# Optimization experiments

Measured on AMD Instinct MI355X. Metric: run time of the kernel, lower is better.

## Reference

```python
import jax, jax.numpy as jnp
import numpy as np

EPS = 1e-8


def setup_inputs() -> dict:
    key = jax.random.key(0)
    k1, k2, k3 = jax.random.split(key, 3)
    B, K, L, D = 4, 64, 128, 768
    context = jax.random.normal(k1, (B, K, 2, L, D), dtype=jnp.float32)
    # MlpModule(input_size=D): Linear(D, D) -> ReLU -> Linear(D, 1)
    w1 = jax.random.normal(k2, (D, D), dtype=jnp.float32) * (1.0 / np.sqrt(D))
    b1 = jnp.zeros((D,), dtype=jnp.float32)
    w2 = jax.random.normal(k3, (D, 1), dtype=jnp.float32) * (1.0 / np.sqrt(D))
    b2 = jnp.zeros((1,), dtype=jnp.float32)
    return {"context": context, "w1": w1, "b1": b1, "w2": w2, "b2": b2}


def reference(context, w1, b1, w2, b2):
    # context: [B, K, 2, L, D]; slice 0 = context tokens, slice 1 = entity tokens
    ctx = context[:, :, 0, :, :]   # [B, K, L, D]
    ent = context[:, :, 1, :, :]   # [B, K, L, D]

    ctx_norm = jnp.linalg.norm(ctx, axis=-1, keepdims=True)  # [B, K, L, 1]
    ent_norm = jnp.linalg.norm(ent, axis=-1, keepdims=True)  # [B, K, L, 1]

    # cosine-similarity score matrix: [B, K, L, L]
    denom = ctx_norm * jnp.swapaxes(ent_norm, -1, -2) + EPS
    scores = jnp.einsum('bkld,bkmd->bklm', ctx, ent) / denom

    # normalized embeddings (torch code does in-place /= before the stack)
    ctx_n = ctx / ctx_norm
    ent_n = ent / ent_norm

    # top-1 match along entity axis, gather matched entity token per context token
    argmax_idx = jnp.argmax(scores, axis=-1)                       # [B, K, L] int
    matched = jnp.take_along_axis(ent_n, argmax_idx[..., None], axis=2)  # [B, K, L, D]

    pair = jnp.stack([ctx_n, matched], axis=-2)  # [B, K, L, 2, D]

    # MLP: Linear(D,D) -> ReLU -> Linear(D,1), then sum over the pair axis
    h = jax.nn.relu(jnp.einsum('bklpd,de->bklpe', pair, w1) + b1)
    out = jnp.einsum('bklpd,do->bklpo', h, w2) + b2   # [B, K, L, 2, 1]
    out = jnp.sum(out, axis=-2)                        # [B, K, L, 1]
    return jnp.squeeze(out, axis=-1)                   # [B, K, L]
```

## Files before the change

kernel.cpp:

```cpp
#include <hip/hip_runtime.h>
#include <hip/hip_bf16.h>
#include <stdint.h>

#define NB 4
#define NK 64
#define NL 128
#define ND 768
#define NBK (NB*NK)
#define NROW (NBK*NL)
#define LD2 (NL*ND)
#define EPSF 1e-8f
#define THETA 2e-3f
#define CAP 16384
#define BTS 56

typedef __bf16 bf16x8 __attribute__((ext_vector_type(8)));
typedef float  f32x4  __attribute__((ext_vector_type(4)));

__device__ __forceinline__ int row_off(int r) {
  if (r < NROW) return r*ND + (r >> 7)*LD2;
  int r2 = r - NROW;
  return r2*ND + (r2 >> 7)*LD2 + LD2;
}

__global__ __launch_bounds__(256) void k0_w1t(const float* __restrict__ w1,
                                              __bf16* __restrict__ w1t,
                                              unsigned long long* __restrict__ amax2,
                                              unsigned* __restrict__ cntg) {
  __shared__ float tile[64][68];
  int idx = blockIdx.x*256 + threadIdx.x;
  if (idx < NROW) amax2[idx] = 0ull;
  if (idx == 0) *cntg = 0u;
  int kb = (blockIdx.x / 12) * 64, eb = (blockIdx.x % 12) * 64;
  int t = threadIdx.x;
  int r = t >> 2, c0 = (t & 3) * 16;
  #pragma unroll
  for (int j = 0; j < 4; j++) {
    f32x4 v = *(const f32x4*)(w1 + (kb + r)*ND + eb + c0 + j*4);
    *(f32x4*)&tile[r][c0 + j*4] = v;
  }
  __syncthreads();
  int e = t & 63, gi = t >> 6;
  int eg = eb + e;
  #pragma unroll
  for (int g2 = 0; g2 < 2; g2++) {
    int g = gi*2 + g2;
    bf16x8 o;
    #pragma unroll
    for (int j = 0; j < 8; j++) o[j] = (__bf16)tile[g*8 + j][e];
    int G = (kb >> 3) + (g ^ (eg & 7));
    *(bf16x8*)(w1t + eg*ND + G*8) = o;
  }
}

__device__ __forceinline__ void cvt4(f32x4 v, unsigned& hp0, unsigned& hp1,
                                     unsigned& lp0, unsigned& lp1, float& sq) {
  unsigned u0 = __float_as_uint(v[0]), u1 = __float_as_uint(v[1]);
  unsigned u2 = __float_as_uint(v[2]), u3 = __float_as_uint(v[3]);
  hp0 = (u1 & 0xffff0000u) | (u0 >> 16);
  hp1 = (u3 & 0xffff0000u) | (u2 >> 16);
  float l0 = v[0] - __uint_as_float(u0 & 0xffff0000u);
  float l1 = v[1] - __uint_as_float(u1 & 0xffff0000u);
  float l2 = v[2] - __uint_as_float(u2 & 0xffff0000u);
  float l3 = v[3] - __uint_as_float(u3 & 0xffff0000u);
  lp0 = (__float_as_uint(l1) & 0xffff0000u) | (__float_as_uint(l0) >> 16);
  lp1 = (__float_as_uint(l3) & 0xffff0000u) | (__float_as_uint(l2) >> 16);
  sq += v[0]*v[0] + v[1]*v[1] + v[2]*v[2] + v[3]*v[3];
}

__global__ __launch_bounds__(256) void k2a_screen(
    const float* __restrict__ ctxall, float* __restrict__ norm,
    int* __restrict__ amax, unsigned* __restrict__ cntg,
    unsigned* __restrict__ list) {
  __shared__ alignas(16) __bf16 Ah[2][64*32], Al[2][64*32];
  __shared__ alignas(16) __bf16 Bh[2][128*BTS], Bl[2][128*BTS];
  __shared__ float einv_s[128];
  int bk = blockIdx.x & 255, half = blockIdx.x >> 8;
  int t = threadIdx.x;
  int w = t >> 6, lane = t & 63, quad = lane >> 4, eloc = lane & 15;
  bool hasA = (t < 128);
  int srow = t >> 1, kh = (t & 1) * 16;
  const float* asrc = ctxall + bk*2*LD2 + (half*64 + srow)*ND + kh;
  const float* bsrc = ctxall + bk*2*LD2 + LD2 + srow*ND + kh;

  f32x4 pa[4], pb[4];
  #pragma unroll
  for (int i = 0; i < 4; i++) pb[i] = *(const f32x4*)(bsrc + i*4);
  if (hasA) {
    #pragma unroll
    for (int i = 0; i < 4; i++) pa[i] = *(const f32x4*)(asrc + i*4);
  }
  float sqa = 0.f, sqb = 0.f;
  f32x4 acc[8];
  #pragma unroll
  for (int ct = 0; ct < 8; ct++) acc[ct] = (f32x4){0,0,0,0};

  int p = 0;
  for (int kt = 0; kt < 24; kt++) {
    unsigned h0,h1,h2,h3, l0,l1,l2,l3;
    cvt4(pb[0], h0, h1, l0, l1, sqb);
    cvt4(pb[1], h2, h3, l2, l3, sqb);
    *(uint4*)&Bh[p][srow*BTS + kh] = make_uint4(h0,h1,h2,h3);
    *(uint4*)&Bl[p][srow*BTS + kh] = make_uint4(l0,l1,l2,l3);
    cvt4(pb[2], h0, h1, l0, l1, sqb);
    cvt4(pb[3], h2, h3, l2, l3, sqb);
    *((uint4*)&Bh[p][srow*BTS + kh] + 1) = make_uint4(h0,h1,h2,h3);
    *((uint4*)&Bl[p][srow*BTS + kh] + 1) = make_uint4(l0,l1,l2,l3);
    if (hasA) {
      cvt4(pa[0], h0, h1, l0, l1, sqa);
      cvt4(pa[1], h2, h3, l2, l3, sqa);
      *(uint4*)&Ah[p][srow*32 + kh] = make_uint4(h0,h1,h2,h3);
      *(uint4*)&Al[p][srow*32 + kh] = make_uint4(l0,l1,l2,l3);
      cvt4(pa[2], h0, h1, l0, l1, sqa);
      cvt4(pa[3], h2, h3, l2, l3, sqa);
      *((uint4*)&Ah[p][srow*32 + kh] + 1) = make_uint4(h0,h1,h2,h3);
      *((uint4*)&Al[p][srow*32 + kh] + 1) = make_uint4(l0,l1,l2,l3);
    }
    __syncthreads();
    if (kt < 23) {
      const float* b2 = bsrc + (kt+1)*32;
      #pragma unroll
      for (int i = 0; i < 4; i++) pb[i] = *(const f32x4*)(b2 + i*4);
      if (hasA) {
        const float* a2 = asrc + (kt+1)*32;
        #pragma unroll
        for (int i = 0; i < 4; i++) pa[i] = *(const f32x4*)(a2 + i*4);
      }
    }
    bf16x8 ah = *(const bf16x8*)&Ah[p][(w*16+eloc)*32 + quad*8];
    bf16x8 al = *(const bf16x8*)&Al[p][(w*16+eloc)*32 + quad*8];
    #pragma unroll
    for (int ct = 0; ct < 8; ct++) {
      bf16x8 bh = *(const bf16x8*)&Bh[p][(ct*16+eloc)*BTS + quad*8];
      bf16x8 bl = *(const bf16x8*)&Bl[p][(ct*16+eloc)*BTS + quad*8];
      acc[ct] = __builtin_amdgcn_mfma_f32_16x16x32_bf16(al, bh, acc[ct], 0, 0, 0);
      acc[ct] = __builtin_amdgcn_mfma_f32_16x16x32_bf16(ah, bl, acc[ct], 0, 0, 0);
      acc[ct] = __builtin_amdgcn_mfma_f32_16x16x32_bf16(ah, bh, acc[ct], 0, 0, 0);
    }
    p ^= 1;
  }

  float stb = sqb + __shfl_xor(sqb, 1);
  if ((t & 1) == 0) {
    float n = sqrtf(stb);
    norm[NROW + bk*NL + srow] = n;
    einv_s[srow] = 1.0f / n;
  }
  if (hasA) {
    float sta = sqa + __shfl_xor(sqa, 1);
    if ((t & 1) == 0) norm[bk*NL + half*64 + srow] = sqrtf(sta);
  }
  __syncthreads();

  #pragma unroll
  for (int rr = 0; rr < 4; rr++) {
    float sc[8];
    float best = -3.0e38f; int bcol = 0;
    #pragma unroll
    for (int ct = 0; ct < 8; ct++) {
      sc[ct] = acc[ct][rr] * einv_s[ct*16 + eloc];
      int col = ct*16 + eloc;
      if (sc[ct] > best) { best = sc[ct]; bcol = col; }
    }
    #pragma unroll
    for (int m = 1; m < 16; m <<= 1) {
      float ov = __shfl_xor(best, m);
      int   oc = __shfl_xor(bcol, m);
      if (ov > best || (ov == best && oc < bcol)) { best = ov; bcol = oc; }
    }
    int grow = bk*NL + half*64 + w*16 + quad*4 + rr;
    if (eloc == 0) amax[grow] = bcol;
    int cnt = 0;
    #pragma unroll
    for (int ct = 0; ct < 8; ct++) cnt += (sc[ct] >= best - THETA) ? 1 : 0;
    #pragma unroll
    for (int m = 1; m < 16; m <<= 1) cnt += __shfl_xor(cnt, m);
    if (cnt >= 2) {
      #pragma unroll
      for (int ct = 0; ct < 8; ct++) {
        if (sc[ct] >= best - THETA) {
          unsigned idx = atomicAdd(cntg, 1u);
          if (idx < CAP) list[idx] = ((unsigned)grow << 7) | (unsigned)(ct*16 + eloc);
        }
      }
    }
  }
}

__global__ __launch_bounds__(256) void k2b_rescore(
    const float* __restrict__ ctxall, const float* __restrict__ norm,
    const unsigned* __restrict__ cntg, const unsigned* __restrict__ list,
    unsigned long long* __restrict__ amax2) {
  unsigned n = *cntg; if (n > CAP) n = CAP;
  int lane = threadIdx.x & 63;
  unsigned wv = blockIdx.x*4 + (threadIdx.x >> 6);
  for (unsigned e = wv; e < n; e += 256) {
    unsigned ent = list[e];
    int row = (int)(ent >> 7), col = (int)(ent & 127);
    int bk = row >> 7;
    const float* a = ctxall + row_off(row);
    const float* b = ctxall + bk*2*LD2 + LD2 + col*ND;
    float d = 0.f;
    #pragma unroll
    for (int i = 0; i < 3; i++) {
      f32x4 va = *(const f32x4*)(a + lane*12 + i*4);
      f32x4 vb = *(const f32x4*)(b + lane*12 + i*4);
      d += va[0]*vb[0] + va[1]*vb[1] + va[2]*vb[2] + va[3]*vb[3];
    }
    #pragma unroll
    for (int m = 1; m < 64; m <<= 1) d += __shfl_xor(d, m);
    if (lane == 0) {
      float cn = norm[row], en = norm[NROW + bk*NL + col];
      float s = d / (cn*en + EPSF);
      unsigned su = __float_as_uint(s);
      unsigned ord = (su & 0x80000000u) ? ~su : (su | 0x80000000u);
      unsigned long long key = ((unsigned long long)ord << 32) | (unsigned)(127 - col);
      atomicMax(&amax2[row], key);
    }
  }
}

__global__ __launch_bounds__(256, 2) void k3_mlp(
    const float* __restrict__ ctxall, const float* __restrict__ norm,
    const __bf16* __restrict__ w1t, const float* __restrict__ b1,
    const float* __restrict__ w2, float* __restrict__ val) {
  __shared__ alignas(16) __bf16 btile[2][16*768];
  int tid = threadIdx.x;
  int wave = tid >> 6, lane = tid & 63;
  int quad = lane >> 4, eloc = lane & 15;
  int rbase = blockIdx.x*128 + wave*32;

  #pragma unroll
  for (int i = 0; i < 6; i++) {
    __builtin_amdgcn_global_load_lds(
      (const __attribute__((address_space(1))) unsigned int*)(w1t + (i*256 + tid)*8),
      (__attribute__((address_space(3))) unsigned int*)(&btile[0][0] + (i*256 + tid)*8),
      16, 0, 0);
  }

  bf16x8 afrag[2][24];
  #pragma unroll
  for (int s = 0; s < 2; s++) {
    int r = rbase + s*16 + eloc;
    const float* src = ctxall + row_off(r);
    float rinv = 1.0f / norm[r];
    #pragma unroll
    for (int ks = 0; ks < 24; ks++) {
      const float* sp = src + ks*32 + quad*8;
      f32x4 v0 = *(const f32x4*)sp;
      f32x4 v1 = *(const f32x4*)(sp + 4);
      bf16x8 a;
      a[0] = (__bf16)(v0[0]*rinv); a[1] = (__bf16)(v0[1]*rinv);
      a[2] = (__bf16)(v0[2]*rinv); a[3] = (__bf16)(v0[3]*rinv);
      a[4] = (__bf16)(v1[0]*rinv); a[5] = (__bf16)(v1[1]*rinv);
      a[6] = (__bf16)(v1[2]*rinv); a[7] = (__bf16)(v1[3]*rinv);
      afrag[s][ks] = a;
    }
  }

  float oacc[2][4] = {{0,0,0,0},{0,0,0,0}};
  int p = 0;
  for (int nt = 0; nt < 48; nt++) {
    __syncthreads();
    if (nt < 47) {
      const __bf16* gsrc = w1t + (nt+1)*16*ND;
      #pragma unroll
      for (int i = 0; i < 6; i++) {
        __builtin_amdgcn_global_load_lds(
          (const __attribute__((address_space(1))) unsigned int*)(gsrc + (i*256 + tid)*8),
          (__attribute__((address_space(3))) unsigned int*)(&btile[p^1][0] + (i*256 + tid)*8),
          16, 0, 0);
      }
    }
    f32x4 h0 = {0,0,0,0}, h1 = {0,0,0,0};
    #pragma unroll
    for (int ks = 0; ks < 24; ks++) {
      int g = ks*4 + quad;
      bf16x8 bfrag = *(const bf16x8*)(&btile[p][0] + eloc*ND + ((g ^ (eloc & 7))*8));
      h0 = __builtin_amdgcn_mfma_f32_16x16x32_bf16(afrag[0][ks], bfrag, h0, 0, 0, 0);
      h1 = __builtin_amdgcn_mfma_f32_16x16x32_bf16(afrag[1][ks], bfrag, h1, 0, 0, 0);
    }
    float b1v = b1[nt*16 + eloc];
    float w2v = w2[nt*16 + eloc];
    #pragma unroll
    for (int rr = 0; rr < 4; rr++) {
      oacc[0][rr] += fmaxf(h0[rr] + b1v, 0.f) * w2v;
      oacc[1][rr] += fmaxf(h1[rr] + b1v, 0.f) * w2v;
    }
    p ^= 1;
  }
  #pragma unroll
  for (int m = 1; m < 16; m <<= 1)
    #pragma unroll
    for (int s = 0; s < 2; s++)
      #pragma unroll
      for (int rr = 0; rr < 4; rr++)
        oacc[s][rr] += __shfl_xor(oacc[s][rr], m);
  if (eloc == 0) {
    #pragma unroll
    for (int s = 0; s < 2; s++)
      #pragma unroll
      for (int rr = 0; rr < 4; rr++)
        val[rbase + s*16 + quad*4 + rr] = oacc[s][rr];
  }
}

__global__ void k4_out(const float* __restrict__ val, const int* __restrict__ amax,
                       const unsigned long long* __restrict__ amax2,
                       const float* __restrict__ b2, float* __restrict__ out) {
  int i = blockIdx.x*256 + threadIdx.x;
  int bk = i >> 7;
  unsigned long long k = amax2[i];
  int a = k ? (127 - (int)(k & 127ull)) : amax[i];
  out[i] = val[i] + val[NROW + bk*NL + a] + 2.0f*b2[0];
}

extern "C" void kernel_launch(void* const* d_in, const int* in_sizes, int n_in,
                              void* d_out, int out_size, void* d_ws, size_t ws_size,
                              hipStream_t stream) {
  const float* ctxall = (const float*)d_in[0];
  const float* w1 = (const float*)d_in[1];
  const float* b1 = (const float*)d_in[2];
  const float* w2 = (const float*)d_in[3];
  const float* b2 = (const float*)d_in[4];
  float* out = (float*)d_out;

  char* ws = (char*)d_ws;
  float*    norm = (float*)ws;
  int*      amax = (int*)(ws + 262144);
  float*    val  = (float*)(ws + 393216);
  __bf16*   w1t  = (__bf16*)(ws + 655360);
  unsigned long long* amax2 = (unsigned long long*)(ws + 1835008);
  unsigned* cntg = (unsigned*)(ws + 2097152);
  unsigned* list = (unsigned*)(ws + 2097156);

  hipLaunchKernelGGL(k0_w1t,     dim3(144),        dim3(256), 0, stream, w1, w1t, amax2, cntg);
  hipLaunchKernelGGL(k2a_screen, dim3(2*NBK),      dim3(256), 0, stream, ctxall, norm, amax, cntg, list);
  hipLaunchKernelGGL(k2b_rescore,dim3(64),         dim3(256), 0, stream, ctxall, norm, cntg, list, amax2);
  hipLaunchKernelGGL(k3_mlp,     dim3(2*NROW/128), dim3(256), 0, stream, ctxall, norm, w1t, b1, w2, val);
  hipLaunchKernelGGL(k4_out,     dim3(NROW/256),   dim3(256), 0, stream, val, amax, amax2, b2, out);
}
```

Measured before the change: 393.6 us.

## Fuse context-row MLP into screening kernel to reuse staged context tiles

The screening kernel grows to 512 threads and, while it stages context rows in LDS for the cosine screen, also runs the first MLP layer for those context rows. It uses a pre-fragmented bf16 copy of W1 that k0 now also writes, and finishes ReLU and the W2 reduction in the same kernel. The standalone MLP kernel then only processes the matched/entity half of rows, so each context row is read from global memory once instead of twice. In exchange the fused kernel carries far more accumulators and register pressure, fetches W1 fragments from global every k-step in every block, and the LDS row stride changes to 40.

```diff
diff --git a/kernel.cpp b/kernel.cpp
--- a/kernel.cpp
+++ b/kernel.cpp
@@ -12,7 +12,7 @@
 #define EPSF 1e-8f
 #define THETA 2e-3f
 #define CAP 16384
-#define BTS 56
+#define TSTR 40
 
 typedef __bf16 bf16x8 __attribute__((ext_vector_type(8)));
 typedef float  f32x4  __attribute__((ext_vector_type(4)));
@@ -25,6 +25,7 @@
 
 __global__ __launch_bounds__(256) void k0_w1t(const float* __restrict__ w1,
                                               __bf16* __restrict__ w1t,
+                                              __bf16* __restrict__ w1f,
                                               unsigned long long* __restrict__ amax2,
                                               unsigned* __restrict__ cntg) {
   __shared__ float tile[64][68];
@@ -50,6 +51,19 @@
     for (int j = 0; j < 8; j++) o[j] = (__bf16)tile[g*8 + j][e];
     int G = (kb >> 3) + (g ^ (eg & 7));
     *(bf16x8*)(w1t + eg*ND + G*8) = o;
+  }
+  #pragma unroll
+  for (int rr = 0; rr < 2; rr++) {
+    int task = t + rr*256;
+    int fi = task >> 6, l = task & 63;
+    int nt_loc = fi & 3, ks_loc = fi >> 2;
+    int quad = l >> 4, eloc = l & 15;
+    bf16x8 o;
+    #pragma unroll
+    for (int j = 0; j < 8; j++)
+      o[j] = (__bf16)tile[ks_loc*32 + quad*8 + j][nt_loc*16 + eloc];
+    int nt = (eb >> 4) + nt_loc, ks = (kb >> 5) + ks_loc;
+    *(bf16x8*)(w1f + (size_t)((nt*24 + ks)*64 + l)*8) = o;
   }
 }
 
@@ -68,122 +82,196 @@
   sq += v[0]*v[0] + v[1]*v[1] + v[2]*v[2] + v[3]*v[3];
 }
 
-__global__ __launch_bounds__(256) void k2a_screen(
+__global__ __launch_bounds__(512, 2) void k2m_fused(
     const float* __restrict__ ctxall, float* __restrict__ norm,
     int* __restrict__ amax, unsigned* __restrict__ cntg,
-    unsigned* __restrict__ list) {
-  __shared__ alignas(16) __bf16 Ah[2][64*32], Al[2][64*32];
-  __shared__ alignas(16) __bf16 Bh[2][128*BTS], Bl[2][128*BTS];
+    unsigned* __restrict__ list, const __bf16* __restrict__ w1f,
+    const float* __restrict__ b1, const float* __restrict__ w2,
+    float* __restrict__ val) {
+  __shared__ alignas(16) __bf16 Bh[2][128*TSTR], Bl[2][128*TSTR];
+  __shared__ alignas(16) __bf16 Ah[2][64*TSTR],  Al[2][64*TSTR];
   __shared__ float einv_s[128];
+  __shared__ float cinv_s[64];
+  __shared__ float red[8][64];
   int bk = blockIdx.x & 255, half = blockIdx.x >> 8;
   int t = threadIdx.x;
   int w = t >> 6, lane = t & 63, quad = lane >> 4, eloc = lane & 15;
-  bool hasA = (t < 128);
-  int srow = t >> 1, kh = (t & 1) * 16;
-  const float* asrc = ctxall + bk*2*LD2 + (half*64 + srow)*ND + kh;
+  bool stE = (t < 256);
+  bool stC = (t >= 256 && t < 384);
+  int srow  = (t >> 1) & 127;
+  int csrow = (t >> 1) & 63;
+  int kh = (t & 1) * 16;
   const float* bsrc = ctxall + bk*2*LD2 + LD2 + srow*ND + kh;
+  const float* asrc = ctxall + bk*2*LD2 + (half*64 + csrow)*ND + kh;
 
   f32x4 pa[4], pb[4];
-  #pragma unroll
-  for (int i = 0; i < 4; i++) pb[i] = *(const f32x4*)(bsrc + i*4);
-  if (hasA) {
+  if (stE) {
+    #pragma unroll
+    for (int i = 0; i < 4; i++) pb[i] = *(const f32x4*)(bsrc + i*4);
+  } else if (stC) {
     #pragma unroll
     for (int i = 0; i < 4; i++) pa[i] = *(const f32x4*)(asrc + i*4);
   }
   float sqa = 0.f, sqb = 0.f;
-  f32x4 acc[8];
-  #pragma unroll
-  for (int ct = 0; ct < 8; ct++) acc[ct] = (f32x4){0,0,0,0};
+  f32x4 accs[8];
+  #pragma unroll
+  for (int ct = 0; ct < 8; ct++) accs[ct] = (f32x4){0,0,0,0};
+  f32x4 accm[6][4];
+  #pragma unroll
+  for (int i = 0; i < 6; i++)
+    #pragma unroll
+    for (int rt = 0; rt < 4; rt++) accm[i][rt] = (f32x4){0,0,0,0};
+  float b1v[6], w2v[6];
+  #pragma unroll
+  for (int i = 0; i < 6; i++) {
+    int c = (w*6 + i)*16 + eloc;
+    b1v[i] = b1[c];
+    w2v[i] = w2[c];
+  }
 
   int p = 0;
   for (int kt = 0; kt < 24; kt++) {
     unsigned h0,h1,h2,h3, l0,l1,l2,l3;
-    cvt4(pb[0], h0, h1, l0, l1, sqb);
-    cvt4(pb[1], h2, h3, l2, l3, sqb);
-    *(uint4*)&Bh[p][srow*BTS + kh] = make_uint4(h0,h1,h2,h3);
-    *(uint4*)&Bl[p][srow*BTS + kh] = make_uint4(l0,l1,l2,l3);
-    cvt4(pb[2], h0, h1, l0, l1, sqb);
-    cvt4(pb[3], h2, h3, l2, l3, sqb);
-    *((uint4*)&Bh[p][srow*BTS + kh] + 1) = make_uint4(h0,h1,h2,h3);
-    *((uint4*)&Bl[p][srow*BTS + kh] + 1) = make_uint4(l0,l1,l2,l3);
-    if (hasA) {
+    if (stE) {
+      cvt4(pb[0], h0, h1, l0, l1, sqb);
+      cvt4(pb[1], h2, h3, l2, l3, sqb);
+      *(uint4*)&Bh[p][srow*TSTR + kh] = make_uint4(h0,h1,h2,h3);
+      *(uint4*)&Bl[p][srow*TSTR + kh] = make_uint4(l0,l1,l2,l3);
+      cvt4(pb[2], h0, h1, l0, l1, sqb);
+      cvt4(pb[3], h2, h3, l2, l3, sqb);
+      *((uint4*)&Bh[p][srow*TSTR + kh] + 1) = make_uint4(h0,h1,h2,h3);
+      *((uint4*)&Bl[p][srow*TSTR + kh] + 1) = make_uint4(l0,l1,l2,l3);
+    } else if (stC) {
       cvt4(pa[0], h0, h1, l0, l1, sqa);
       cvt4(pa[1], h2, h3, l2, l3, sqa);
-      *(uint4*)&Ah[p][srow*32 + kh] = make_uint4(h0,h1,h2,h3);
-      *(uint4*)&Al[p][srow*32 + kh] = make_uint4(l0,l1,l2,l3);
+      *(uint4*)&Ah[p][csrow*TSTR + kh] = make_uint4(h0,h1,h2,h3);
+      *(uint4*)&Al[p][csrow*TSTR + kh] = make_uint4(l0,l1,l2,l3);
       cvt4(pa[2], h0, h1, l0, l1, sqa);
       cvt4(pa[3], h2, h3, l2, l3, sqa);
-      *((uint4*)&Ah[p][srow*32 + kh] + 1) = make_uint4(h0,h1,h2,h3);
-      *((uint4*)&Al[p][srow*32 + kh] + 1) = make_uint4(l0,l1,l2,l3);
+      *((uint4*)&Ah[p][csrow*TSTR + kh] + 1) = make_uint4(h0,h1,h2,h3);
+      *((uint4*)&Al[p][csrow*TSTR + kh] + 1) = make_uint4(l0,l1,l2,l3);
     }
     __syncthreads();
+    bf16x8 bf[6];
+    #pragma unroll
+    for (int i = 0; i < 6; i++)
+      bf[i] = *(const bf16x8*)(w1f + (size_t)(((w*6 + i)*24 + kt)*64 + lane)*8);
     if (kt < 23) {
-      const float* b2 = bsrc + (kt+1)*32;
-      #pragma unroll
-      for (int i = 0; i < 4; i++) pb[i] = *(const f32x4*)(b2 + i*4);
-      if (hasA) {
-        const float* a2 = asrc + (kt+1)*32;
+      if (stE) {
+        const float* b2p = bsrc + (kt+1)*32;
         #pragma unroll
-        for (int i = 0; i < 4; i++) pa[i] = *(const f32x4*)(a2 + i*4);
-      }
-    }
-    bf16x8 ah = *(const bf16x8*)&Ah[p][(w*16+eloc)*32 + quad*8];
-    bf16x8 al = *(const bf16x8*)&Al[p][(w*16+eloc)*32 + quad*8];
-    #pragma unroll
-    for (int ct = 0; ct < 8; ct++) {
-      bf16x8 bh = *(const bf16x8*)&Bh[p][(ct*16+eloc)*BTS + quad*8];
-      bf16x8 bl = *(const bf16x8*)&Bl[p][(ct*16+eloc)*BTS + quad*8];
-      acc[ct] = __builtin_amdgcn_mfma_f32_16x16x32_bf16(al, bh, acc[ct], 0, 0, 0);
-      acc[ct] = __builtin_amdgcn_mfma_f32_16x16x32_bf16(ah, bl, acc[ct], 0, 0, 0);
-      acc[ct] = __builtin_amdgcn_mfma_f32_16x16x32_bf16(ah, bh, acc[ct], 0, 0, 0);
+        for (int i = 0; i < 4; i++) pb[i] = *(const f32x4*)(b2p + i*4);
+      } else if (stC) {
+        const float* a2p = asrc + (kt+1)*32;
+        #pragma unroll
+        for (int i = 0; i < 4; i++) pa[i] = *(const f32x4*)(a2p + i*4);
+      }
+    }
+    if (t < 256) {
+      bf16x8 ah = *(const bf16x8*)&Ah[p][(w*16+eloc)*TSTR + quad*8];
+      bf16x8 al = *(const bf16x8*)&Al[p][(w*16+eloc)*TSTR + quad*8];
+      #pragma unroll
+      for (int ct = 0; ct < 8; ct++) {
+        bf16x8 bh = *(const bf16x8*)&Bh[p][(ct*16+eloc)*TSTR + quad*8];
+        bf16x8 bl = *(const bf16x8*)&Bl[p][(ct*16+eloc)*TSTR + quad*8];
+        accs[ct] = __builtin_amdgcn_mfma_f32_16x16x32_bf16(al, bh, accs[ct], 0, 0, 0);
+        accs[ct] = __builtin_amdgcn_mfma_f32_16x16x32_bf16(ah, bl, accs[ct], 0, 0, 0);
+        accs[ct] = __builtin_amdgcn_mfma_f32_16x16x32_bf16(ah, bh, accs[ct], 0, 0, 0);
+      }
+    }
+    #pragma unroll
+    for (int rt = 0; rt < 4; rt++) {
+      bf16x8 mah = *(const bf16x8*)&Ah[p][(rt*16+eloc)*TSTR + quad*8];
+      bf16x8 mal = *(const bf16x8*)&Al[p][(rt*16+eloc)*TSTR + quad*8];
+      #pragma unroll
+      for (int i = 0; i < 6; i++) {
+        accm[i][rt] = __builtin_amdgcn_mfma_f32_16x16x32_bf16(mal, bf[i], accm[i][rt], 0, 0, 0);
+        accm[i][rt] = __builtin_amdgcn_mfma_f32_16x16x32_bf16(mah, bf[i], accm[i][rt], 0, 0, 0);
+      }
     }
     p ^= 1;
   }
 
-  float stb = sqb + __shfl_xor(sqb, 1);
-  if ((t & 1) == 0) {
-    float n = sqrtf(stb);
-    norm[NROW + bk*NL + srow] = n;
-    einv_s[srow] = 1.0f / n;
-  }
-  if (hasA) {
+  if (stE) {
+    float stb = sqb + __shfl_xor(sqb, 1);
+    if ((t & 1) == 0) {
+      float n = sqrtf(stb);
+      norm[NROW + bk*NL + srow] = n;
+      einv_s[srow] = 1.0f / n;
+    }
+  } else if (stC) {
     float sta = sqa + __shfl_xor(sqa, 1);
-    if ((t & 1) == 0) norm[bk*NL + half*64 + srow] = sqrtf(sta);
+    if ((t & 1) == 0) {
+      float n = sqrtf(sta);
+      norm[bk*NL + half*64 + csrow] = n;
+      cinv_s[csrow] = 1.0f / n;
+    }
   }
   __syncthreads();
 
-  #pragma unroll
-  for (int rr = 0; rr < 4; rr++) {
-    float sc[8];
-    float best = -3.0e38f; int bcol = 0;
-    #pragma unroll
-    for (int ct = 0; ct < 8; ct++) {
-      sc[ct] = acc[ct][rr] * einv_s[ct*16 + eloc];
-      int col = ct*16 + eloc;
-      if (sc[ct] > best) { best = sc[ct]; bcol = col; }
-    }
-    #pragma unroll
-    for (int m = 1; m < 16; m <<= 1) {
-      float ov = __shfl_xor(best, m);
-      int   oc = __shfl_xor(bcol, m);
-      if (ov > best || (ov == best && oc < bcol)) { best = ov; bcol = oc; }
-    }
-    int grow = bk*NL + half*64 + w*16 + quad*4 + rr;
-    if (eloc == 0) amax[grow] = bcol;
-    int cnt = 0;
-    #pragma unroll
-    for (int ct = 0; ct < 8; ct++) cnt += (sc[ct] >= best - THETA) ? 1 : 0;
-    #pragma unroll
-    for (int m = 1; m < 16; m <<= 1) cnt += __shfl_xor(cnt, m);
-    if (cnt >= 2) {
+  if (t < 256) {
+    #pragma unroll
+    for (int rr = 0; rr < 4; rr++) {
+      float sc[8];
+      float best = -3.0e38f; int bcol = 0;
       #pragma unroll
       for (int ct = 0; ct < 8; ct++) {
-        if (sc[ct] >= best - THETA) {
-          unsigned idx = atomicAdd(cntg, 1u);
-          if (idx < CAP) list[idx] = ((unsigned)grow << 7) | (unsigned)(ct*16 + eloc);
+        sc[ct] = accs[ct][rr] * einv_s[ct*16 + eloc];
+        int col = ct*16 + eloc;
+        if (sc[ct] > best) { best = sc[ct]; bcol = col; }
+      }
+      #pragma unroll
+      for (int m = 1; m < 16; m <<= 1) {
+        float ov = __shfl_xor(best, m);
+        int   oc = __shfl_xor(bcol, m);
+        if (ov > best || (ov == best && oc < bcol)) { best = ov; bcol = oc; }
+      }
+      int grow = bk*NL + half*64 + w*16 + quad*4 + rr;
+      if (eloc == 0) amax[grow] = bcol;
+      int cnt = 0;
+      #pragma unroll
+      for (int ct = 0; ct < 8; ct++) cnt += (sc[ct] >= best - THETA) ? 1 : 0;
+      #pragma unroll
+      for (int m = 1; m < 16; m <<= 1) cnt += __shfl_xor(cnt, m);
+      if (cnt >= 2) {
+        #pragma unroll
+        for (int ct = 0; ct < 8; ct++) {
+          if (sc[ct] >= best - THETA) {
+            unsigned idx = atomicAdd(cntg, 1u);
+            if (idx < CAP) list[idx] = ((unsigned)grow << 7) | (unsigned)(ct*16 + eloc);
+          }
         }
       }
     }
+  }
+
+  #pragma unroll
+  for (int rt = 0; rt < 4; rt++) {
+    float pr[4];
+    #pragma unroll
+    for (int rr = 0; rr < 4; rr++) {
+      float ci = cinv_s[rt*16 + quad*4 + rr];
+      float s = 0.f;
+      #pragma unroll
+      for (int i = 0; i < 6; i++)
+        s += fmaxf(accm[i][rt][rr]*ci + b1v[i], 0.f) * w2v[i];
+      pr[rr] = s;
+    }
+    #pragma unroll
+    for (int m = 1; m < 16; m <<= 1)
+      #pragma unroll
+      for (int rr = 0; rr < 4; rr++) pr[rr] += __shfl_xor(pr[rr], m);
+    if (eloc == 0) {
+      #pragma unroll
+      for (int rr = 0; rr < 4; rr++) red[w][rt*16 + quad*4 + rr] = pr[rr];
+    }
+  }
+  __syncthreads();
+  if (t < 64) {
+    float s = 0.f;
+    #pragma unroll
+    for (int w8 = 0; w8 < 8; w8++) s += red[w8][t];
+    val[bk*NL + half*64 + t] = s;
   }
 }
 
@@ -223,12 +311,12 @@
 __global__ __launch_bounds__(256, 2) void k3_mlp(
     const float* __restrict__ ctxall, const float* __restrict__ norm,
     const __bf16* __restrict__ w1t, const float* __restrict__ b1,
-    const float* __restrict__ w2, float* __restrict__ val) {
+    const float* __restrict__ w2, float* __restrict__ val, int rb0) {
   __shared__ alignas(16) __bf16 btile[2][16*768];
   int tid = threadIdx.x;
   int wave = tid >> 6, lane = tid & 63;
   int quad = lane >> 4, eloc = lane & 15;
-  int rbase = blockIdx.x*128 + wave*32;
+  int rbase = rb0 + blockIdx.x*128 + wave*32;
 
   #pragma unroll
   for (int i = 0; i < 6; i++) {
@@ -333,10 +421,11 @@
   unsigned long long* amax2 = (unsigned long long*)(ws + 1835008);
   unsigned* cntg = (unsigned*)(ws + 2097152);
   unsigned* list = (unsigned*)(ws + 2097156);
-
-  hipLaunchKernelGGL(k0_w1t,     dim3(144),        dim3(256), 0, stream, w1, w1t, amax2, cntg);
-  hipLaunchKernelGGL(k2a_screen, dim3(2*NBK),      dim3(256), 0, stream, ctxall, norm, amax, cntg, list);
-  hipLaunchKernelGGL(k2b_rescore,dim3(64),         dim3(256), 0, stream, ctxall, norm, cntg, list, amax2);
-  hipLaunchKernelGGL(k3_mlp,     dim3(2*NROW/128), dim3(256), 0, stream, ctxall, norm, w1t, b1, w2, val);
-  hipLaunchKernelGGL(k4_out,     dim3(NROW/256),   dim3(256), 0, stream, val, amax, amax2, b2, out);
-}
+  __bf16*   w1f  = (__bf16*)(ws + 2228224);
+
+  hipLaunchKernelGGL(k0_w1t,     dim3(144),      dim3(256), 0, stream, w1, w1t, w1f, amax2, cntg);
+  hipLaunchKernelGGL(k2m_fused,  dim3(2*NBK),    dim3(512), 0, stream, ctxall, norm, amax, cntg, list, w1f, b1, w2, val);
+  hipLaunchKernelGGL(k2b_rescore,dim3(64),       dim3(256), 0, stream, ctxall, norm, cntg, list, amax2);
+  hipLaunchKernelGGL(k3_mlp,     dim3(NROW/128), dim3(256), 0, stream, ctxall, norm, w1t, b1, w2, val, NROW);
+  hipLaunchKernelGGL(k4_out,     dim3(NROW/256), dim3(256), 0, stream, val, amax, amax2, b2, out);
+}
```

Measured after the change: 428.1 us. 8.8% more time.
